# Kernel tuning notes

Measured on AMD Instinct MI355X. Metric: run time of the kernel, lower is better.

The kernel has to match this reference:

```python
import jax, jax.numpy as jnp
import numpy as np

N_NODES = 100000
N_EDGES = 1600000
N_PAIRS = 200000
IN_CH = 128
HID_CH = 128


def _graph_conv(x, src, dst, edge_weight, w_rel, b_rel, w_root, num_nodes):
    # PyG GraphConv with aggr='mean':
    # out = lin_rel(mean_{j in N(i)}(x_j * w_ij)) + lin_root(x_i)
    msg = x[src] * edge_weight[:, None]                       # [E, C] gather
    agg = jax.ops.segment_sum(msg, dst, num_segments=num_nodes)  # [N, C]
    cnt = jax.ops.segment_sum(jnp.ones((src.shape[0],), x.dtype), dst,
                              num_segments=num_nodes)          # in-degree
    agg = agg / jnp.maximum(cnt, 1.0)[:, None]                 # mean aggr
    return agg @ w_rel + b_rel + x @ w_root


def setup_inputs() -> dict:
    key = jax.random.key(0)
    ks = jax.random.split(key, 10)
    x = jax.random.normal(ks[0], (N_NODES, IN_CH), dtype=jnp.float32)
    edge_index = jax.random.randint(ks[1], (2, N_EDGES), 0, N_NODES, dtype=jnp.int32)
    edge_weight = jax.random.uniform(ks[2], (N_EDGES,), dtype=jnp.float32)
    edge_label_index = jax.random.randint(ks[3], (2, N_PAIRS), 0, N_NODES, dtype=jnp.int32)
    s1 = 1.0 / np.sqrt(IN_CH)
    s2 = 1.0 / np.sqrt(HID_CH)
    w1_rel = jax.random.uniform(ks[4], (IN_CH, HID_CH), jnp.float32, -s1, s1)
    b1_rel = jnp.zeros((HID_CH,), jnp.float32)
    w1_root = jax.random.uniform(ks[5], (IN_CH, HID_CH), jnp.float32, -s1, s1)
    w2_rel = jax.random.uniform(ks[6], (HID_CH, HID_CH), jnp.float32, -s2, s2)
    b2_rel = jnp.zeros((HID_CH,), jnp.float32)
    w2_root = jax.random.uniform(ks[7], (HID_CH, HID_CH), jnp.float32, -s2, s2)
    return {"x": x, "edge_index": edge_index, "edge_weight": edge_weight,
            "edge_label_index": edge_label_index,
            "w1_rel": w1_rel, "b1_rel": b1_rel, "w1_root": w1_root,
            "w2_rel": w2_rel, "b2_rel": b2_rel, "w2_root": w2_root}


def reference(x, edge_index, edge_weight, edge_label_index,
              w1_rel, b1_rel, w1_root, w2_rel, b2_rel, w2_root):
    src, dst = edge_index[0], edge_index[1]
    # encode
    h = _graph_conv(x, src, dst, edge_weight, w1_rel, b1_rel, w1_root, x.shape[0])
    h = jax.nn.relu(h)
    z = _graph_conv(h, src, dst, edge_weight, w2_rel, b2_rel, w2_root, x.shape[0])
    # decode: scaled dot product between candidate pair embeddings
    zs = z[edge_label_index[0]]   # [P, H]
    zd = z[edge_label_index[1]]   # [P, H]
    scale = z.shape[-1] ** 0.5
    return jnp.sum(zs * zd, axis=-1) / scale
```

## Files before the change

kernel.cpp:

```cpp
#include <hip/hip_runtime.h>

#define NN 100000
#define NE 1600000
#define NP 200000
#define CH 128
#define LK 264

#define BSH 6
#define NB  1563
#define G1  256
#define EPB (NE / G1)
#define CAP3 4096
#define NCAST 6250
#define CSG 25

typedef _Float16 f16x8 __attribute__((ext_vector_type(8)));
typedef _Float16 f16x4 __attribute__((ext_vector_type(4)));
typedef float f32x4 __attribute__((ext_vector_type(4)));

__global__ __launch_bounds__(256)
void fused_prep_kernel(const float* __restrict__ x, _Float16* __restrict__ xh,
                       const int* __restrict__ dst, int* __restrict__ hist,
                       const float* __restrict__ w1r, const float* __restrict__ w1o,
                       const float* __restrict__ w2r, const float* __restrict__ w2o,
                       _Float16* __restrict__ w1t, _Float16* __restrict__ w2t,
                       int* __restrict__ sync) {
    __shared__ int s_h[NB];
    const int bb = blockIdx.x, tid = threadIdx.x;
    if (bb < NCAST) {
        int i = bb * 256 + tid;
        const float4* p = (const float4*)x + (size_t)i * 2;
        float4 a = p[0], b = p[1];
        f16x8 o = { (_Float16)a.x, (_Float16)a.y, (_Float16)a.z, (_Float16)a.w,
                    (_Float16)b.x, (_Float16)b.y, (_Float16)b.z, (_Float16)b.w };
        *((f16x8*)xh + i) = o;
    } else if (bb < NCAST + G1) {
        int g = bb - NCAST;
        for (int i = tid; i < NB; i += 256) s_h[i] = 0;
        __syncthreads();
        int start = g * EPB, end = start + EPB;
        for (int e = start + tid; e < end; e += 256)
            atomicAdd(&s_h[dst[e] >> BSH], 1);
        __syncthreads();
        int* row = hist + (size_t)g * NB;
        for (int i = tid; i < NB; i += 256) row[i] = s_h[i];
    } else {
        int idx = (bb - NCAST - G1) * 256 + tid;
        if (idx == 0) *sync = 0;
        int which = idx >> 15;
        int li = idx & 32767;
        int n = li >> 8, k = li & 255;
        const float* wr = which ? w2r : w1r;
        const float* wo = which ? w2o : w1o;
        _Float16* wt = which ? w2t : w1t;
        float v = (k < 128) ? wr[k * 128 + n] : wo[(k - 128) * 128 + n];
        wt[li] = (_Float16)v;
    }
}

__global__ __launch_bounds__(256)
void colscan_kernel(int* __restrict__ hist, int* __restrict__ totals,
                    int* __restrict__ base, int* __restrict__ sync) {
    __shared__ int qs[4][64];
    __shared__ int s_sync;
    __shared__ int ws[4];
    const int tid = threadIdx.x;
    const int q = tid >> 6, lb = tid & 63;
    const int b = blockIdx.x * 64 + lb;
    const bool valid = (b < NB);

    int s = 0;
    if (valid) {
        for (int g = q * 64; g < q * 64 + 64; ++g)
            s += hist[(size_t)g * NB + b];
    }
    qs[q][lb] = s;
    __syncthreads();

    if (tid < 64) {
        int a0 = qs[0][tid], a1 = qs[1][tid], a2 = qs[2][tid], a3 = qs[3][tid];
        qs[0][tid] = 0;
        qs[1][tid] = a0;
        qs[2][tid] = a0 + a1;
        qs[3][tid] = a0 + a1 + a2;
        int bt = blockIdx.x * 64 + tid;
        if (bt < NB) totals[bt] = a0 + a1 + a2 + a3;
    }
    __syncthreads();

    int run = qs[q][lb];
    if (valid) {
        for (int g = q * 64; g < q * 64 + 64; ++g) {
            size_t idx = (size_t)g * NB + b;
            int v = hist[idx];
            hist[idx] = run;
            run += v;
        }
    }

    __syncthreads();
    if (tid == 0) {
        __threadfence();
        s_sync = atomicAdd(sync, 1);
    }
    __syncthreads();
    if (s_sync != CSG - 1) return;
    __threadfence();

    const int c0 = tid * 7;
    int incl7[7];
    int cs = 0;
#pragma unroll
    for (int k = 0; k < 7; k++) {
        int i = c0 + k;
        int t = (i < NB) ? totals[i] : 0;
        cs += t;
        incl7[k] = cs;
    }
    int lane = tid & 63, w = tid >> 6;
    int incl = cs;
#pragma unroll
    for (int off = 1; off < 64; off <<= 1) {
        int n = __shfl_up(incl, off, 64);
        if (lane >= off) incl += n;
    }
    if (lane == 63) ws[w] = incl;
    __syncthreads();
    int woff = 0;
    for (int j = 0; j < w; j++) woff += ws[j];
    int chunk_excl = woff + incl - cs;
    if (tid == 0) base[0] = 0;
#pragma unroll
    for (int k = 0; k < 7; k++) {
        int i = c0 + k;
        if (i < NB) base[i + 1] = chunk_excl + incl7[k];
    }
}

__global__ __launch_bounds__(512)
void bucket_scatter_kernel(const int* __restrict__ src, const int* __restrict__ dst,
                           const float* __restrict__ ew, const int* __restrict__ hist,
                           const int* __restrict__ base, int2* __restrict__ tmp) {
    __shared__ int s_cur[NB];
    const int* row = hist + (size_t)blockIdx.x * NB;
    for (int i = threadIdx.x; i < NB; i += 512) s_cur[i] = base[i] + row[i];
    __syncthreads();
    int start = blockIdx.x * EPB, end = start + EPB;
    for (int e = start + threadIdx.x; e < end; e += 512) {
        int d = dst[e];
        int b = d >> BSH;
        int pos = atomicAdd(&s_cur[b], 1);
        tmp[pos] = make_int2(src[e] | ((d & 63) << 17), __float_as_int(ew[e]));
    }
}

__global__ __launch_bounds__(512)
void bucket_finalize_kernel(const int2* __restrict__ tmp, const int* __restrict__ base,
                            int* __restrict__ row_ptr, int2* __restrict__ csr, int N) {
    __shared__ int2 s_e[CAP3];
    __shared__ int s_cnt[64], s_off[64];
    int b = blockIdx.x;
    int lo = base[b], hi = base[b + 1];
    int size = hi - lo;
    int nbase = b << BSH;
    int ncnt = min(64, N - nbase);
    int tid = threadIdx.x;
    if (tid < 64) s_cnt[tid] = 0;
    bool inlds = (size <= CAP3);
    __syncthreads();
    if (inlds) {
        for (int i = tid; i < size; i += 512) {
            int2 e = tmp[lo + i];
            s_e[i] = e;
            atomicAdd(&s_cnt[(e.x >> 17) & 63], 1);
        }
    } else {
        for (int i = tid; i < size; i += 512) {
            int2 e = tmp[lo + i];
            atomicAdd(&s_cnt[(e.x >> 17) & 63], 1);
        }
    }
    __syncthreads();
    if (tid < 64) {
        int v = s_cnt[tid];
        int incl = v;
#pragma unroll
        for (int off = 1; off < 64; off <<= 1) {
            int n = __shfl_up(incl, off, 64);
            if (tid >= off) incl += n;
        }
        int excl = incl - v;
        s_off[tid] = excl;
        s_cnt[tid] = excl;
    }
    __syncthreads();
    if (tid < ncnt) row_ptr[nbase + tid] = lo + s_off[tid];
    if (b == NB - 1 && tid == 0) row_ptr[N] = hi;
    if (inlds) {
        for (int i = tid; i < size; i += 512) {
            int2 e = s_e[i];
            int dl = (e.x >> 17) & 63;
            int p = atomicAdd(&s_cnt[dl], 1);
            csr[lo + p] = make_int2(e.x & 0x1FFFF, e.y);
        }
    } else {
        for (int i = tid; i < size; i += 512) {
            int2 e = tmp[lo + i];
            int dl = (e.x >> 17) & 63;
            int p = atomicAdd(&s_cnt[dl], 1);
            csr[lo + p] = make_int2(e.x & 0x1FFFF, e.y);
        }
    }
}

template <bool RELU>
__global__ __launch_bounds__(512)
void gatherlayer_kernel(const _Float16* __restrict__ feat, const int* __restrict__ row_ptr,
                        const int2* __restrict__ csr, const _Float16* __restrict__ wt,
                        const float* __restrict__ bias, _Float16* __restrict__ out, int N) {
    __shared__ _Float16 atile[64][LK];

    const int tid = threadIdx.x;
    const int nb = blockIdx.x << BSH;
    const int wave = tid >> 6;
    const int lane = tid & 63;
    const int q = lane >> 4;
    const int l16 = lane & 15;
    const int c8 = l16 << 3;

    for (int nn = 0; nn < 8; nn++) {
        int local_n = wave * 8 + nn;
        int node = nb + local_n;
        if (node >= N) break;
        int r0 = row_ptr[node], r1 = row_ptr[node + 1];
        float acc[8] = {0.f, 0.f, 0.f, 0.f, 0.f, 0.f, 0.f, 0.f};
        int r = r0 + q;
        if (r < r1) {
            int2 e = csr[r];
            f16x8 v = *(const f16x8*)&feat[(size_t)e.x * CH + c8];
            int2 e2; f16x8 v2;
            bool h2 = (r + 4) < r1;
            if (h2) { e2 = csr[r + 4]; v2 = *(const f16x8*)&feat[(size_t)e2.x * CH + c8]; }
            for (int r3 = r + 8; r3 < r1; r3 += 4) {
                int2 e3 = csr[r3];
                f16x8 v3 = *(const f16x8*)&feat[(size_t)e3.x * CH + c8];
                float w = __int_as_float(e.y);
#pragma unroll
                for (int j = 0; j < 8; j++) acc[j] += w * (float)v[j];
                e = e2; v = v2;
                e2 = e3; v2 = v3;
            }
            float w = __int_as_float(e.y);
#pragma unroll
            for (int j = 0; j < 8; j++) acc[j] += w * (float)v[j];
            if (h2) {
                float w2 = __int_as_float(e2.y);
#pragma unroll
                for (int j = 0; j < 8; j++) acc[j] += w2 * (float)v2[j];
            }
        }
#pragma unroll
        for (int j = 0; j < 8; j++) {
            acc[j] += __shfl_xor(acc[j], 16, 64);
            acc[j] += __shfl_xor(acc[j], 32, 64);
        }
        if (q == 0) {
            float inv = 1.0f / fmaxf((float)(r1 - r0), 1.0f);
            f16x8 o;
#pragma unroll
            for (int j = 0; j < 8; j++) o[j] = (_Float16)(acc[j] * inv);
            *(f16x8*)&atile[local_n][c8] = o;
        }
    }

    for (int i = tid; i < 64 * 16; i += 512) {
        int rrow = i >> 4;
        int cc8 = (i & 15) << 3;
        int gn = nb + rrow;
        f16x8 v = {};
        if (gn < N) v = *(const f16x8*)&feat[(size_t)gn * CH + cc8];
        *(f16x8*)&atile[rrow][128 + cc8] = v;
    }
    __syncthreads();

    f32x4 ac[4];
#pragma unroll
    for (int m = 0; m < 4; m++) ac[m] = (f32x4){0.f, 0.f, 0.f, 0.f};

    const int ncol = wave * 16 + l16;
    const int kq = q * 8;
#pragma unroll
    for (int ks = 0; ks < 8; ks++) {
        int kbase = ks * 32 + kq;
        f16x8 bf = *(const f16x8*)&wt[(size_t)ncol * 256 + kbase];
#pragma unroll
        for (int m = 0; m < 4; m++) {
            f16x8 af = *(const f16x8*)&atile[m * 16 + l16][kbase];
            ac[m] = __builtin_amdgcn_mfma_f32_16x16x32_f16(af, bf, ac[m], 0, 0, 0);
        }
    }

    float bv = bias[ncol];
#pragma unroll
    for (int m = 0; m < 4; m++) {
#pragma unroll
        for (int r = 0; r < 4; r++) {
            int node = nb + m * 16 + q * 4 + r;
            if (node >= N) continue;
            float v = ac[m][r] + bv;
            if (RELU) v = fmaxf(v, 0.f);
            out[(size_t)node * CH + ncol] = (_Float16)v;
        }
    }
}

__global__ void decode_kernel(const _Float16* __restrict__ z,
                              const int* __restrict__ ps,
                              const int* __restrict__ pd,
                              float* __restrict__ out, int P) {
    long tid = (long)blockIdx.x * blockDim.x + threadIdx.x;
    int p = (int)(tid >> 5);
    int lane32 = (int)(tid & 31);
    if (p >= P) return;
    int l16 = lane32 & 15;
    int half = lane32 >> 4;
    int row = half ? pd[p] : ps[p];
    int4 a = *(const int4*)&z[(size_t)row * CH + l16 * 8];
    int4 b;
    b.x = __shfl_xor(a.x, 16, 64);
    b.y = __shfl_xor(a.y, 16, 64);
    b.z = __shfl_xor(a.z, 16, 64);
    b.w = __shfl_xor(a.w, 16, 64);
    union U { int4 i; f16x8 h; };
    U ua, ub; ua.i = a; ub.i = b;
    float v = 0.f;
#pragma unroll
    for (int j = 0; j < 8; j++) v += (float)ua.h[j] * (float)ub.h[j];
#pragma unroll
    for (int off = 8; off > 0; off >>= 1) v += __shfl_xor(v, off, 64);
    if (lane32 == 0) out[p] = v * 0.08838834764831845f;
}

extern "C" void kernel_launch(void* const* d_in, const int* in_sizes, int n_in,
                              void* d_out, int out_size, void* d_ws, size_t ws_size,
                              hipStream_t stream) {
    const float* x       = (const float*)d_in[0];
    const int*   ei      = (const int*)d_in[1];
    const float* ew      = (const float*)d_in[2];
    const int*   eli     = (const int*)d_in[3];
    const float* w1_rel  = (const float*)d_in[4];
    const float* b1      = (const float*)d_in[5];
    const float* w1_root = (const float*)d_in[6];
    const float* w2_rel  = (const float*)d_in[7];
    const float* b2      = (const float*)d_in[8];
    const float* w2_root = (const float*)d_in[9];
    float* out = (float*)d_out;

    const int N = NN, E = NE, P = NP;
    const size_t hrow = (size_t)N * CH * sizeof(_Float16);

    char* ws = (char*)d_ws;
    size_t off = 0;
    auto alloc = [&](size_t bytes) { char* p = ws + off; off = (off + bytes + 15) & ~(size_t)15; return p; };
    _Float16* xh  = (_Float16*)alloc(hrow);
    _Float16* hh  = (_Float16*)alloc(hrow);
    _Float16* zh  = (_Float16*)alloc(hrow);
    int* hist     = (int*)alloc((size_t)G1 * NB * 4);
    int* totals   = (int*)alloc((size_t)NB * 4);
    int* base     = (int*)alloc((size_t)(NB + 1) * 4);
    int* row_ptr  = (int*)alloc((size_t)(N + 1) * 4);
    int* sync     = (int*)alloc(16);
    int2* tmp     = (int2*)alloc((size_t)E * 8);
    int2* csr     = (int2*)alloc((size_t)E * 8);
    _Float16* w1t = (_Float16*)alloc((size_t)128 * 256 * 2);
    _Float16* w2t = (_Float16*)alloc((size_t)128 * 256 * 2);

    const int* src = ei;
    const int* dst = ei + E;

    fused_prep_kernel<<<NCAST + G1 + 256, 256, 0, stream>>>(
        x, xh, dst, hist, w1_rel, w1_root, w2_rel, w2_root, w1t, w2t, sync);

    colscan_kernel<<<CSG, 256, 0, stream>>>(hist, totals, base, sync);
    bucket_scatter_kernel<<<G1, 512, 0, stream>>>(src, dst, ew, hist, base, tmp);
    bucket_finalize_kernel<<<NB, 512, 0, stream>>>(tmp, base, row_ptr, csr, N);

    gatherlayer_kernel<true><<<NB, 512, 0, stream>>>(xh, row_ptr, csr, w1t, b1, hh, N);
    gatherlayer_kernel<false><<<NB, 512, 0, stream>>>(hh, row_ptr, csr, w2t, b2, zh, N);

    {
        long threads = (long)P * 32;
        decode_kernel<<<(int)((threads + 255) / 256), 256, 0, stream>>>(zh, eli, eli + P, out, P);
    }
}
```

Baseline: 371.1 us.

## Fuse all stages into one cooperative persistent kernel with grid syncs

Replaces the seven separate kernel launches with one persistent cooperative kernel. Its grid is sized from occupancy, and grid.sync() separates the cast/histogram, column scan, scatter, CSR finalize, the two gather-GEMM layers and decode. The aim is to remove launch gaps and tail effects between stages. In exchange the grid is capped at 1024 blocks, the histogram partition is rescaled to that grid, grid-wide barriers are added, and each block runs a strided loop over work. The later stages may lose occupancy or latency hiding compared with the original one-block-per-bucket grids.

```diff
diff --git a/kernel.cpp b/kernel.cpp
--- a/kernel.cpp
+++ b/kernel.cpp
@@ -1,4 +1,7 @@
 #include <hip/hip_runtime.h>
+#include <hip/hip_cooperative_groups.h>
+
+namespace cg = cooperative_groups;
 
 #define NN 100000
 #define NE 1600000
@@ -8,47 +11,50 @@
 
 #define BSH 6
 #define NB  1563
-#define G1  256
-#define EPB (NE / G1)
 #define CAP3 4096
-#define NCAST 6250
-#define CSG 25
+#define CSB 25
+#define SMEM_BYTES 33792
+#define MAXGB 1024
 
 typedef _Float16 f16x8 __attribute__((ext_vector_type(8)));
-typedef _Float16 f16x4 __attribute__((ext_vector_type(4)));
 typedef float f32x4 __attribute__((ext_vector_type(4)));
 
-__global__ __launch_bounds__(256)
-void fused_prep_kernel(const float* __restrict__ x, _Float16* __restrict__ xh,
-                       const int* __restrict__ dst, int* __restrict__ hist,
-                       const float* __restrict__ w1r, const float* __restrict__ w1o,
-                       const float* __restrict__ w2r, const float* __restrict__ w2o,
-                       _Float16* __restrict__ w1t, _Float16* __restrict__ w2t,
-                       int* __restrict__ sync) {
-    __shared__ int s_h[NB];
-    const int bb = blockIdx.x, tid = threadIdx.x;
-    if (bb < NCAST) {
-        int i = bb * 256 + tid;
+struct Params {
+    const float* x; const int* src; const int* dst; const float* ew;
+    const int* ps; const int* pd;
+    const float* w1r; const float* b1; const float* w1o;
+    const float* w2r; const float* b2; const float* w2o;
+    _Float16* xh; _Float16* hh; _Float16* zh;
+    int* hist; int* totals; int* base; int* row_ptr; int* syncc;
+    int2* tmp; int2* csr;
+    _Float16* w1t; _Float16* w2t;
+    float* out;
+};
+
+__device__ __forceinline__ void edge_range(int bid, int GB, int& st, int& cnt) {
+    int epb = NE / GB, rem = NE % GB;
+    st = bid * epb + min(bid, rem);
+    cnt = epb + (bid < rem ? 1 : 0);
+}
+
+__device__ __forceinline__ void d_cast(const float* __restrict__ x, _Float16* __restrict__ xh,
+                                       int gid, int gstride) {
+    for (int i = gid; i < NN * CH / 8; i += gstride) {
         const float4* p = (const float4*)x + (size_t)i * 2;
         float4 a = p[0], b = p[1];
         f16x8 o = { (_Float16)a.x, (_Float16)a.y, (_Float16)a.z, (_Float16)a.w,
                     (_Float16)b.x, (_Float16)b.y, (_Float16)b.z, (_Float16)b.w };
         *((f16x8*)xh + i) = o;
-    } else if (bb < NCAST + G1) {
-        int g = bb - NCAST;
-        for (int i = tid; i < NB; i += 256) s_h[i] = 0;
-        __syncthreads();
-        int start = g * EPB, end = start + EPB;
-        for (int e = start + tid; e < end; e += 256)
-            atomicAdd(&s_h[dst[e] >> BSH], 1);
-        __syncthreads();
-        int* row = hist + (size_t)g * NB;
-        for (int i = tid; i < NB; i += 256) row[i] = s_h[i];
-    } else {
-        int idx = (bb - NCAST - G1) * 256 + tid;
-        if (idx == 0) *sync = 0;
-        int which = idx >> 15;
-        int li = idx & 32767;
+    }
+}
+
+__device__ __forceinline__ void d_weights(const float* __restrict__ w1r, const float* __restrict__ w1o,
+                                          const float* __restrict__ w2r, const float* __restrict__ w2o,
+                                          _Float16* __restrict__ w1t, _Float16* __restrict__ w2t,
+                                          int gid) {
+    if (gid < 65536) {
+        int which = gid >> 15;
+        int li = gid & 32767;
         int n = li >> 8, k = li & 255;
         const float* wr = which ? w2r : w1r;
         const float* wo = which ? w2o : w1o;
@@ -58,39 +64,55 @@
     }
 }
 
-__global__ __launch_bounds__(256)
-void colscan_kernel(int* __restrict__ hist, int* __restrict__ totals,
-                    int* __restrict__ base, int* __restrict__ sync) {
-    __shared__ int qs[4][64];
-    __shared__ int s_sync;
-    __shared__ int ws[4];
-    const int tid = threadIdx.x;
-    const int q = tid >> 6, lb = tid & 63;
-    const int b = blockIdx.x * 64 + lb;
+__device__ __forceinline__ void d_hist(const int* __restrict__ dst, int* __restrict__ hist,
+                                       int bid, int GB, int tid, void* smem) {
+    int* s_h = (int*)smem;
+    for (int i = tid; i < NB; i += 512) s_h[i] = 0;
+    __syncthreads();
+    int st, cnt; edge_range(bid, GB, st, cnt);
+    for (int e = st + tid; e < st + cnt; e += 512)
+        atomicAdd(&s_h[dst[e] >> BSH], 1);
+    __syncthreads();
+    int* row = hist + (size_t)bid * NB;
+    for (int i = tid; i < NB; i += 512) row[i] = s_h[i];
+    __syncthreads();
+}
+
+__device__ __forceinline__ void d_colscan(int* __restrict__ hist, int* __restrict__ totals,
+                                          int* __restrict__ base, int* __restrict__ syncc,
+                                          int bid, int GB, int tid, void* smem) {
+    if (bid >= CSB) return;
+    int* qs = (int*)smem;
+    int* ws = qs + 512;
+    int* s_sync = ws + 8;
+    const int c = tid >> 6, lb = tid & 63;
+    const int b = bid * 64 + lb;
     const bool valid = (b < NB);
+    const int rows = GB >> 3;
 
     int s = 0;
+    if (valid)
+        for (int g = c * rows; g < (c + 1) * rows; ++g)
+            s += hist[(size_t)g * NB + b];
+    qs[c * 64 + lb] = s;
+    __syncthreads();
+
+    if (tid < 64) {
+        int a[8], tot = 0;
+#pragma unroll
+        for (int j = 0; j < 8; j++) a[j] = qs[j * 64 + tid];
+        int run = 0;
+#pragma unroll
+        for (int j = 0; j < 8; j++) { qs[j * 64 + tid] = run; run += a[j]; }
+        tot = run;
+        int bt = bid * 64 + tid;
+        if (bt < NB) totals[bt] = tot;
+    }
+    __syncthreads();
+
+    int run = qs[c * 64 + lb];
     if (valid) {
-        for (int g = q * 64; g < q * 64 + 64; ++g)
-            s += hist[(size_t)g * NB + b];
-    }
-    qs[q][lb] = s;
-    __syncthreads();
-
-    if (tid < 64) {
-        int a0 = qs[0][tid], a1 = qs[1][tid], a2 = qs[2][tid], a3 = qs[3][tid];
-        qs[0][tid] = 0;
-        qs[1][tid] = a0;
-        qs[2][tid] = a0 + a1;
-        qs[3][tid] = a0 + a1 + a2;
-        int bt = blockIdx.x * 64 + tid;
-        if (bt < NB) totals[bt] = a0 + a1 + a2 + a3;
-    }
-    __syncthreads();
-
-    int run = qs[q][lb];
-    if (valid) {
-        for (int g = q * 64; g < q * 64 + 64; ++g) {
+        for (int g = c * rows; g < (c + 1) * rows; ++g) {
             size_t idx = (size_t)g * NB + b;
             int v = hist[idx];
             hist[idx] = run;
@@ -101,21 +123,21 @@
     __syncthreads();
     if (tid == 0) {
         __threadfence();
-        s_sync = atomicAdd(sync, 1);
-    }
-    __syncthreads();
-    if (s_sync != CSG - 1) return;
+        *s_sync = atomicAdd(syncc, 1);
+    }
+    __syncthreads();
+    if (*s_sync != CSB - 1) return;
     __threadfence();
 
-    const int c0 = tid * 7;
-    int incl7[7];
+    const int c0 = tid * 4;
+    int incl4[4];
     int cs = 0;
 #pragma unroll
-    for (int k = 0; k < 7; k++) {
+    for (int k = 0; k < 4; k++) {
         int i = c0 + k;
         int t = (i < NB) ? totals[i] : 0;
         cs += t;
-        incl7[k] = cs;
+        incl4[k] = cs;
     }
     int lane = tid & 63, w = tid >> 6;
     int incl = cs;
@@ -131,40 +153,40 @@
     int chunk_excl = woff + incl - cs;
     if (tid == 0) base[0] = 0;
 #pragma unroll
-    for (int k = 0; k < 7; k++) {
+    for (int k = 0; k < 4; k++) {
         int i = c0 + k;
-        if (i < NB) base[i + 1] = chunk_excl + incl7[k];
-    }
-}
-
-__global__ __launch_bounds__(512)
-void bucket_scatter_kernel(const int* __restrict__ src, const int* __restrict__ dst,
-                           const float* __restrict__ ew, const int* __restrict__ hist,
-                           const int* __restrict__ base, int2* __restrict__ tmp) {
-    __shared__ int s_cur[NB];
-    const int* row = hist + (size_t)blockIdx.x * NB;
-    for (int i = threadIdx.x; i < NB; i += 512) s_cur[i] = base[i] + row[i];
-    __syncthreads();
-    int start = blockIdx.x * EPB, end = start + EPB;
-    for (int e = start + threadIdx.x; e < end; e += 512) {
+        if (i < NB) base[i + 1] = chunk_excl + incl4[k];
+    }
+}
+
+__device__ __forceinline__ void d_scatter(const int* __restrict__ src, const int* __restrict__ dst,
+                                          const float* __restrict__ ew, const int* __restrict__ hist,
+                                          const int* __restrict__ base, int2* __restrict__ tmp,
+                                          int bid, int GB, int tid, void* smem) {
+    int* s_cur = (int*)smem;
+    const int* row = hist + (size_t)bid * NB;
+    for (int i = tid; i < NB; i += 512) s_cur[i] = base[i] + row[i];
+    __syncthreads();
+    int st, cnt; edge_range(bid, GB, st, cnt);
+    for (int e = st + tid; e < st + cnt; e += 512) {
         int d = dst[e];
         int b = d >> BSH;
         int pos = atomicAdd(&s_cur[b], 1);
         tmp[pos] = make_int2(src[e] | ((d & 63) << 17), __float_as_int(ew[e]));
     }
-}
-
-__global__ __launch_bounds__(512)
-void bucket_finalize_kernel(const int2* __restrict__ tmp, const int* __restrict__ base,
-                            int* __restrict__ row_ptr, int2* __restrict__ csr, int N) {
-    __shared__ int2 s_e[CAP3];
-    __shared__ int s_cnt[64], s_off[64];
-    int b = blockIdx.x;
+    __syncthreads();
+}
+
+__device__ __forceinline__ void d_finalize(const int2* __restrict__ tmp, const int* __restrict__ base,
+                                           int* __restrict__ row_ptr, int2* __restrict__ csr,
+                                           int b, int tid, void* smem) {
+    int2* s_e = (int2*)smem;
+    int* s_cnt = (int*)((char*)smem + 32768);
+    int* s_off = s_cnt + 64;
     int lo = base[b], hi = base[b + 1];
     int size = hi - lo;
     int nbase = b << BSH;
-    int ncnt = min(64, N - nbase);
-    int tid = threadIdx.x;
+    int ncnt = min(64, NN - nbase);
     if (tid < 64) s_cnt[tid] = 0;
     bool inlds = (size <= CAP3);
     __syncthreads();
@@ -195,7 +217,7 @@
     }
     __syncthreads();
     if (tid < ncnt) row_ptr[nbase + tid] = lo + s_off[tid];
-    if (b == NB - 1 && tid == 0) row_ptr[N] = hi;
+    if (b == NB - 1 && tid == 0) row_ptr[NN] = hi;
     if (inlds) {
         for (int i = tid; i < size; i += 512) {
             int2 e = s_e[i];
@@ -214,14 +236,12 @@
 }
 
 template <bool RELU>
-__global__ __launch_bounds__(512)
-void gatherlayer_kernel(const _Float16* __restrict__ feat, const int* __restrict__ row_ptr,
-                        const int2* __restrict__ csr, const _Float16* __restrict__ wt,
-                        const float* __restrict__ bias, _Float16* __restrict__ out, int N) {
-    __shared__ _Float16 atile[64][LK];
-
-    const int tid = threadIdx.x;
-    const int nb = blockIdx.x << BSH;
+__device__ __forceinline__ void d_gather(const _Float16* __restrict__ feat, const int* __restrict__ row_ptr,
+                                         const int2* __restrict__ csr, const _Float16* __restrict__ wt,
+                                         const float* __restrict__ bias, _Float16* __restrict__ out,
+                                         int bk, int tid, void* smem) {
+    _Float16 (*atile)[LK] = (_Float16(*)[LK])smem;
+    const int nb = bk << BSH;
     const int wave = tid >> 6;
     const int lane = tid & 63;
     const int q = lane >> 4;
@@ -231,7 +251,7 @@
     for (int nn = 0; nn < 8; nn++) {
         int local_n = wave * 8 + nn;
         int node = nb + local_n;
-        if (node >= N) break;
+        if (node >= NN) break;
         int r0 = row_ptr[node], r1 = row_ptr[node + 1];
         float acc[8] = {0.f, 0.f, 0.f, 0.f, 0.f, 0.f, 0.f, 0.f};
         int r = r0 + q;
@@ -278,7 +298,7 @@
         int cc8 = (i & 15) << 3;
         int gn = nb + rrow;
         f16x8 v = {};
-        if (gn < N) v = *(const f16x8*)&feat[(size_t)gn * CH + cc8];
+        if (gn < NN) v = *(const f16x8*)&feat[(size_t)gn * CH + cc8];
         *(f16x8*)&atile[rrow][128 + cc8] = v;
     }
     __syncthreads();
@@ -306,7 +326,7 @@
 #pragma unroll
         for (int r = 0; r < 4; r++) {
             int node = nb + m * 16 + q * 4 + r;
-            if (node >= N) continue;
+            if (node >= NN) continue;
             float v = ac[m][r] + bv;
             if (RELU) v = fmaxf(v, 0.f);
             out[(size_t)node * CH + ncol] = (_Float16)v;
@@ -314,31 +334,112 @@
     }
 }
 
-__global__ void decode_kernel(const _Float16* __restrict__ z,
-                              const int* __restrict__ ps,
-                              const int* __restrict__ pd,
-                              float* __restrict__ out, int P) {
-    long tid = (long)blockIdx.x * blockDim.x + threadIdx.x;
-    int p = (int)(tid >> 5);
-    int lane32 = (int)(tid & 31);
-    if (p >= P) return;
+__device__ __forceinline__ void d_decode(const _Float16* __restrict__ z,
+                                         const int* __restrict__ ps, const int* __restrict__ pd,
+                                         float* __restrict__ out, int gid, int gstride) {
+    int lane32 = gid & 31;
     int l16 = lane32 & 15;
     int half = lane32 >> 4;
-    int row = half ? pd[p] : ps[p];
-    int4 a = *(const int4*)&z[(size_t)row * CH + l16 * 8];
-    int4 b;
-    b.x = __shfl_xor(a.x, 16, 64);
-    b.y = __shfl_xor(a.y, 16, 64);
-    b.z = __shfl_xor(a.z, 16, 64);
-    b.w = __shfl_xor(a.w, 16, 64);
-    union U { int4 i; f16x8 h; };
-    U ua, ub; ua.i = a; ub.i = b;
-    float v = 0.f;
-#pragma unroll
-    for (int j = 0; j < 8; j++) v += (float)ua.h[j] * (float)ub.h[j];
-#pragma unroll
-    for (int off = 8; off > 0; off >>= 1) v += __shfl_xor(v, off, 64);
-    if (lane32 == 0) out[p] = v * 0.08838834764831845f;
+    for (int p = gid >> 5; p < NP; p += (gstride >> 5)) {
+        int row = half ? pd[p] : ps[p];
+        int4 a = *(const int4*)&z[(size_t)row * CH + l16 * 8];
+        int4 b;
+        b.x = __shfl_xor(a.x, 16, 64);
+        b.y = __shfl_xor(a.y, 16, 64);
+        b.z = __shfl_xor(a.z, 16, 64);
+        b.w = __shfl_xor(a.w, 16, 64);
+        union U { int4 i; f16x8 h; };
+        U ua, ub; ua.i = a; ub.i = b;
+        float v = 0.f;
+#pragma unroll
+        for (int j = 0; j < 8; j++) v += (float)ua.h[j] * (float)ub.h[j];
+#pragma unroll
+        for (int off = 8; off > 0; off >>= 1) v += __shfl_xor(v, off, 64);
+        if (lane32 == 0) out[p] = v * 0.08838834764831845f;
+    }
+}
+
+__global__ __launch_bounds__(512, 8)
+void mono_kernel(Params P, int GB) {
+    __shared__ alignas(16) unsigned char smem[SMEM_BYTES];
+    cg::grid_group grid = cg::this_grid();
+    const int bid = blockIdx.x, tid = threadIdx.x;
+    const int gid = bid * 512 + tid, gstride = GB * 512;
+
+    d_cast(P.x, P.xh, gid, gstride);
+    d_weights(P.w1r, P.w1o, P.w2r, P.w2o, P.w1t, P.w2t, gid);
+    if (gid == 0) *P.syncc = 0;
+    d_hist(P.dst, P.hist, bid, GB, tid, smem);
+    grid.sync();
+
+    d_colscan(P.hist, P.totals, P.base, P.syncc, bid, GB, tid, smem);
+    grid.sync();
+
+    d_scatter(P.src, P.dst, P.ew, P.hist, P.base, P.tmp, bid, GB, tid, smem);
+    grid.sync();
+
+    for (int b = bid; b < NB; b += GB) {
+        __syncthreads();
+        d_finalize(P.tmp, P.base, P.row_ptr, P.csr, b, tid, smem);
+    }
+    grid.sync();
+
+    for (int b = bid; b < NB; b += GB) {
+        __syncthreads();
+        d_gather<true>(P.xh, P.row_ptr, P.csr, P.w1t, P.b1, P.hh, b, tid, smem);
+    }
+    grid.sync();
+
+    for (int b = bid; b < NB; b += GB) {
+        __syncthreads();
+        d_gather<false>(P.hh, P.row_ptr, P.csr, P.w2t, P.b2, P.zh, b, tid, smem);
+    }
+    grid.sync();
+
+    d_decode(P.zh, P.ps, P.pd, P.out, gid, gstride);
+}
+
+__global__ __launch_bounds__(512) void k_p1(Params P, int GB) {
+    __shared__ alignas(16) unsigned char smem[SMEM_BYTES];
+    const int bid = blockIdx.x, tid = threadIdx.x;
+    const int gid = bid * 512 + tid, gstride = GB * 512;
+    d_cast(P.x, P.xh, gid, gstride);
+    d_weights(P.w1r, P.w1o, P.w2r, P.w2o, P.w1t, P.w2t, gid);
+    if (gid == 0) *P.syncc = 0;
+    d_hist(P.dst, P.hist, bid, GB, tid, smem);
+}
+__global__ __launch_bounds__(512) void k_p2(Params P, int GB) {
+    __shared__ alignas(16) unsigned char smem[SMEM_BYTES];
+    d_colscan(P.hist, P.totals, P.base, P.syncc, blockIdx.x, GB, threadIdx.x, smem);
+}
+__global__ __launch_bounds__(512) void k_p3(Params P, int GB) {
+    __shared__ alignas(16) unsigned char smem[SMEM_BYTES];
+    d_scatter(P.src, P.dst, P.ew, P.hist, P.base, P.tmp, blockIdx.x, GB, threadIdx.x, smem);
+}
+__global__ __launch_bounds__(512) void k_p4(Params P, int GB) {
+    __shared__ alignas(16) unsigned char smem[SMEM_BYTES];
+    for (int b = blockIdx.x; b < NB; b += GB) {
+        __syncthreads();
+        d_finalize(P.tmp, P.base, P.row_ptr, P.csr, b, threadIdx.x, smem);
+    }
+}
+__global__ __launch_bounds__(512) void k_p5(Params P, int GB) {
+    __shared__ alignas(16) unsigned char smem[SMEM_BYTES];
+    for (int b = blockIdx.x; b < NB; b += GB) {
+        __syncthreads();
+        d_gather<true>(P.xh, P.row_ptr, P.csr, P.w1t, P.b1, P.hh, b, threadIdx.x, smem);
+    }
+}
+__global__ __launch_bounds__(512) void k_p6(Params P, int GB) {
+    __shared__ alignas(16) unsigned char smem[SMEM_BYTES];
+    for (int b = blockIdx.x; b < NB; b += GB) {
+        __syncthreads();
+        d_gather<false>(P.hh, P.row_ptr, P.csr, P.w2t, P.b2, P.zh, b, threadIdx.x, smem);
+    }
+}
+__global__ __launch_bounds__(512) void k_p7(Params P, int GB) {
+    const int gid = blockIdx.x * 512 + threadIdx.x;
+    d_decode(P.zh, P.ps, P.pd, P.out, gid, GB * 512);
 }
 
 extern "C" void kernel_launch(void* const* d_in, const int* in_sizes, int n_in,
@@ -354,42 +455,53 @@
     const float* w2_rel  = (const float*)d_in[7];
     const float* b2      = (const float*)d_in[8];
     const float* w2_root = (const float*)d_in[9];
-    float* out = (float*)d_out;
-
-    const int N = NN, E = NE, P = NP;
-    const size_t hrow = (size_t)N * CH * sizeof(_Float16);
+
+    const size_t hrow = (size_t)NN * CH * sizeof(_Float16);
 
     char* ws = (char*)d_ws;
     size_t off = 0;
     auto alloc = [&](size_t bytes) { char* p = ws + off; off = (off + bytes + 15) & ~(size_t)15; return p; };
-    _Float16* xh  = (_Float16*)alloc(hrow);
-    _Float16* hh  = (_Float16*)alloc(hrow);
-    _Float16* zh  = (_Float16*)alloc(hrow);
-    int* hist     = (int*)alloc((size_t)G1 * NB * 4);
-    int* totals   = (int*)alloc((size_t)NB * 4);
-    int* base     = (int*)alloc((size_t)(NB + 1) * 4);
-    int* row_ptr  = (int*)alloc((size_t)(N + 1) * 4);
-    int* sync     = (int*)alloc(16);
-    int2* tmp     = (int2*)alloc((size_t)E * 8);
-    int2* csr     = (int2*)alloc((size_t)E * 8);
-    _Float16* w1t = (_Float16*)alloc((size_t)128 * 256 * 2);
-    _Float16* w2t = (_Float16*)alloc((size_t)128 * 256 * 2);
-
-    const int* src = ei;
-    const int* dst = ei + E;
-
-    fused_prep_kernel<<<NCAST + G1 + 256, 256, 0, stream>>>(
-        x, xh, dst, hist, w1_rel, w1_root, w2_rel, w2_root, w1t, w2t, sync);
-
-    colscan_kernel<<<CSG, 256, 0, stream>>>(hist, totals, base, sync);
-    bucket_scatter_kernel<<<G1, 512, 0, stream>>>(src, dst, ew, hist, base, tmp);
-    bucket_finalize_kernel<<<NB, 512, 0, stream>>>(tmp, base, row_ptr, csr, N);
-
-    gatherlayer_kernel<true><<<NB, 512, 0, stream>>>(xh, row_ptr, csr, w1t, b1, hh, N);
-    gatherlayer_kernel<false><<<NB, 512, 0, stream>>>(hh, row_ptr, csr, w2t, b2, zh, N);
-
-    {
-        long threads = (long)P * 32;
-        decode_kernel<<<(int)((threads + 255) / 256), 256, 0, stream>>>(zh, eli, eli + P, out, P);
-    }
-}
+    Params P;
+    P.xh      = (_Float16*)alloc(hrow);
+    P.hh      = (_Float16*)alloc(hrow);
+    P.zh      = (_Float16*)alloc(hrow);
+    P.hist    = (int*)alloc((size_t)MAXGB * NB * 4);
+    P.totals  = (int*)alloc((size_t)NB * 4);
+    P.base    = (int*)alloc((size_t)(NB + 1) * 4);
+    P.row_ptr = (int*)alloc((size_t)(NN + 1) * 4);
+    P.syncc   = (int*)alloc(16);
+    P.tmp     = (int2*)alloc((size_t)NE * 8);
+    P.csr     = (int2*)alloc((size_t)NE * 8);
+    P.w1t     = (_Float16*)alloc((size_t)128 * 256 * 2);
+    P.w2t     = (_Float16*)alloc((size_t)128 * 256 * 2);
+
+    P.x = x; P.src = ei; P.dst = ei + NE; P.ew = ew;
+    P.ps = eli; P.pd = eli + NP;
+    P.w1r = w1_rel; P.b1 = b1; P.w1o = w1_root;
+    P.w2r = w2_rel; P.b2 = b2; P.w2o = w2_root;
+    P.out = (float*)d_out;
+
+    int maxb = 0;
+    hipError_t qe = hipOccupancyMaxActiveBlocksPerMultiprocessor(&maxb, (const void*)mono_kernel, 512, 0);
+    int GB = (qe == hipSuccess && maxb > 0) ? maxb * 256 : MAXGB;
+    if (GB > MAXGB) GB = MAXGB;
+    GB &= ~7;
+
+    bool coop_ok = (GB >= 64);
+    if (coop_ok) {
+        void* args[] = { (void*)&P, (void*)&GB };
+        hipError_t e = hipLaunchCooperativeKernel((const void*)mono_kernel, dim3(GB), dim3(512),
+                                                  args, 0, stream);
+        if (e != hipSuccess) { (void)hipGetLastError(); coop_ok = false; }
+    }
+    if (!coop_ok) {
+        int GBF = MAXGB;
+        k_p1<<<GBF, 512, 0, stream>>>(P, GBF);
+        k_p2<<<CSB, 512, 0, stream>>>(P, GBF);
+        k_p3<<<GBF, 512, 0, stream>>>(P, GBF);
+        k_p4<<<GBF, 512, 0, stream>>>(P, GBF);
+        k_p5<<<GBF, 512, 0, stream>>>(P, GBF);
+        k_p6<<<GBF, 512, 0, stream>>>(P, GBF);
+        k_p7<<<GBF, 512, 0, stream>>>(P, GBF);
+    }
+}
```

Result: slower. 834.5 us (+124.9%).

## Fuse bucket finalize with first-layer gather and MFMA transform

Applied to the files above, without the earlier changes.

Merges the CSR bucket finalize kernel with the layer-1 gather/aggregate/GEMM kernel, so each block builds its 64-node CSR segment and immediately aggregates and transforms those nodes. The LDS edge buffer and the A tile share storage through a union, and row offsets come from shared memory instead of a global row_ptr read. This removes one kernel launch and the re-read of row_ptr. The csr entries just written are still read back through global memory, and the larger LDS footprint may lower occupancy.

```diff
diff --git a/kernel.cpp b/kernel.cpp
--- a/kernel.cpp
+++ b/kernel.cpp
@@ -15,7 +15,6 @@
 #define CSG 25
 
 typedef _Float16 f16x8 __attribute__((ext_vector_type(8)));
-typedef _Float16 f16x4 __attribute__((ext_vector_type(4)));
 typedef float f32x4 __attribute__((ext_vector_type(4)));
 
 __global__ __launch_bounds__(256)
@@ -155,23 +154,30 @@
 }
 
 __global__ __launch_bounds__(512)
-void bucket_finalize_kernel(const int2* __restrict__ tmp, const int* __restrict__ base,
-                            int* __restrict__ row_ptr, int2* __restrict__ csr, int N) {
-    __shared__ int2 s_e[CAP3];
-    __shared__ int s_cnt[64], s_off[64];
-    int b = blockIdx.x;
-    int lo = base[b], hi = base[b + 1];
-    int size = hi - lo;
-    int nbase = b << BSH;
-    int ncnt = min(64, N - nbase);
-    int tid = threadIdx.x;
+void finalize_gather1_kernel(const int2* __restrict__ tmp, const int* __restrict__ base,
+                             int* __restrict__ row_ptr, int2* __restrict__ csr,
+                             const _Float16* __restrict__ feat, const _Float16* __restrict__ wt,
+                             const float* __restrict__ bias, _Float16* __restrict__ out, int N) {
+    __shared__ union alignas(16) {
+        int2 s_e[CAP3];
+        _Float16 atile[64][LK];
+    } u;
+    __shared__ int s_cnt[64], s_off[65];
+
+    const int b = blockIdx.x;
+    const int tid = threadIdx.x;
+    const int lo = base[b], hi = base[b + 1];
+    const int size = hi - lo;
+    const int nbase = b << BSH;
+    const int ncnt = min(64, N - nbase);
+
     if (tid < 64) s_cnt[tid] = 0;
     bool inlds = (size <= CAP3);
     __syncthreads();
     if (inlds) {
         for (int i = tid; i < size; i += 512) {
             int2 e = tmp[lo + i];
-            s_e[i] = e;
+            u.s_e[i] = e;
             atomicAdd(&s_cnt[(e.x >> 17) & 63], 1);
         }
     } else {
@@ -192,13 +198,14 @@
         int excl = incl - v;
         s_off[tid] = excl;
         s_cnt[tid] = excl;
+        if (tid == 63) s_off[64] = incl;
     }
     __syncthreads();
     if (tid < ncnt) row_ptr[nbase + tid] = lo + s_off[tid];
     if (b == NB - 1 && tid == 0) row_ptr[N] = hi;
     if (inlds) {
         for (int i = tid; i < size; i += 512) {
-            int2 e = s_e[i];
+            int2 e = u.s_e[i];
             int dl = (e.x >> 17) & 63;
             int p = atomicAdd(&s_cnt[dl], 1);
             csr[lo + p] = make_int2(e.x & 0x1FFFF, e.y);
@@ -209,6 +216,98 @@
             int dl = (e.x >> 17) & 63;
             int p = atomicAdd(&s_cnt[dl], 1);
             csr[lo + p] = make_int2(e.x & 0x1FFFF, e.y);
+        }
+    }
+    __syncthreads();
+
+    const int wave = tid >> 6;
+    const int lane = tid & 63;
+    const int q = lane >> 4;
+    const int l16 = lane & 15;
+    const int c8 = l16 << 3;
+
+    for (int nn = 0; nn < 8; nn++) {
+        int local_n = wave * 8 + nn;
+        int node = nbase + local_n;
+        if (node >= N) break;
+        int r0 = lo + s_off[local_n], r1 = lo + s_off[local_n + 1];
+        float acc[8] = {0.f, 0.f, 0.f, 0.f, 0.f, 0.f, 0.f, 0.f};
+        int r = r0 + q;
+        if (r < r1) {
+            int2 e = csr[r];
+            f16x8 v = *(const f16x8*)&feat[(size_t)e.x * CH + c8];
+            int2 e2; f16x8 v2;
+            bool h2 = (r + 4) < r1;
+            if (h2) { e2 = csr[r + 4]; v2 = *(const f16x8*)&feat[(size_t)e2.x * CH + c8]; }
+            for (int r3 = r + 8; r3 < r1; r3 += 4) {
+                int2 e3 = csr[r3];
+                f16x8 v3 = *(const f16x8*)&feat[(size_t)e3.x * CH + c8];
+                float w = __int_as_float(e.y);
+#pragma unroll
+                for (int j = 0; j < 8; j++) acc[j] += w * (float)v[j];
+                e = e2; v = v2;
+                e2 = e3; v2 = v3;
+            }
+            float w = __int_as_float(e.y);
+#pragma unroll
+            for (int j = 0; j < 8; j++) acc[j] += w * (float)v[j];
+            if (h2) {
+                float w2 = __int_as_float(e2.y);
+#pragma unroll
+                for (int j = 0; j < 8; j++) acc[j] += w2 * (float)v2[j];
+            }
+        }
+#pragma unroll
+        for (int j = 0; j < 8; j++) {
+            acc[j] += __shfl_xor(acc[j], 16, 64);
+            acc[j] += __shfl_xor(acc[j], 32, 64);
+        }
+        if (q == 0) {
+            float inv = 1.0f / fmaxf((float)(r1 - r0), 1.0f);
+            f16x8 o;
+#pragma unroll
+            for (int j = 0; j < 8; j++) o[j] = (_Float16)(acc[j] * inv);
+            *(f16x8*)&u.atile[local_n][c8] = o;
+        }
+    }
+
+    for (int i = tid; i < 64 * 16; i += 512) {
+        int rrow = i >> 4;
+        int cc8 = (i & 15) << 3;
+        int gn = nbase + rrow;
+        f16x8 v = {};
+        if (gn < N) v = *(const f16x8*)&feat[(size_t)gn * CH + cc8];
+        *(f16x8*)&u.atile[rrow][128 + cc8] = v;
+    }
+    __syncthreads();
+
+    f32x4 ac[4];
+#pragma unroll
+    for (int m = 0; m < 4; m++) ac[m] = (f32x4){0.f, 0.f, 0.f, 0.f};
+
+    const int ncol = wave * 16 + l16;
+    const int kq = q * 8;
+#pragma unroll
+    for (int ks = 0; ks < 8; ks++) {
+        int kbase = ks * 32 + kq;
+        f16x8 bf = *(const f16x8*)&wt[(size_t)ncol * 256 + kbase];
+#pragma unroll
+        for (int m = 0; m < 4; m++) {
+            f16x8 af = *(const f16x8*)&u.atile[m * 16 + l16][kbase];
+            ac[m] = __builtin_amdgcn_mfma_f32_16x16x32_f16(af, bf, ac[m], 0, 0, 0);
+        }
+    }
+
+    float bv = bias[ncol];
+#pragma unroll
+    for (int m = 0; m < 4; m++) {
+#pragma unroll
+        for (int r = 0; r < 4; r++) {
+            int node = nbase + m * 16 + q * 4 + r;
+            if (node >= N) continue;
+            float v = ac[m][r] + bv;
+            v = fmaxf(v, 0.f);
+            out[(size_t)node * CH + ncol] = (_Float16)v;
         }
     }
 }
@@ -383,9 +482,10 @@
 
     colscan_kernel<<<CSG, 256, 0, stream>>>(hist, totals, base, sync);
     bucket_scatter_kernel<<<G1, 512, 0, stream>>>(src, dst, ew, hist, base, tmp);
-    bucket_finalize_kernel<<<NB, 512, 0, stream>>>(tmp, base, row_ptr, csr, N);
-
-    gatherlayer_kernel<true><<<NB, 512, 0, stream>>>(xh, row_ptr, csr, w1t, b1, hh, N);
+
+    finalize_gather1_kernel<<<NB, 512, 0, stream>>>(tmp, base, row_ptr, csr,
+                                                    xh, w1t, b1, hh, N);
+
     gatherlayer_kernel<false><<<NB, 512, 0, stream>>>(hh, row_ptr, csr, w2t, b2, zh, N);
 
     {
```

After: 367.6 us. No clear change (-0.9%).
